# Kernel optimization log

Hardware: AMD Instinct MI355X
Metric: run time of the kernel (lower is better)

The kernel has to match this reference:

```python
import jax, jax.numpy as jnp
import numpy as np

D_MODEL = 1024
N_HEADS = 16
D_HEAD = D_MODEL // N_HEADS


def setup_inputs() -> dict:
    key = jax.random.key(0)
    ks = jax.random.split(key, 9)
    s = 1.0 / np.sqrt(D_MODEL)
    x = jax.random.normal(ks[0], (2, 2048, D_MODEL), dtype=jnp.float32)
    # torch nn.Linear stores weight [out, in]; we store [in, out] for x @ W
    Wq = jax.random.uniform(ks[1], (D_MODEL, D_MODEL), jnp.float32, -s, s)
    bq = jax.random.uniform(ks[2], (D_MODEL,), jnp.float32, -s, s)
    Wk = jax.random.uniform(ks[3], (D_MODEL, D_MODEL), jnp.float32, -s, s)
    bk = jax.random.uniform(ks[4], (D_MODEL,), jnp.float32, -s, s)
    Wv = jax.random.uniform(ks[5], (D_MODEL, D_MODEL), jnp.float32, -s, s)
    bv = jax.random.uniform(ks[6], (D_MODEL,), jnp.float32, -s, s)
    Wo = jax.random.uniform(ks[7], (D_MODEL, D_MODEL), jnp.float32, -s, s)
    bo = jax.random.uniform(ks[8], (D_MODEL,), jnp.float32, -s, s)
    return {"x": x, "Wq": Wq, "bq": bq, "Wk": Wk, "bk": bk,
            "Wv": Wv, "bv": bv, "Wo": Wo, "bo": bo}


def reference(x, Wq, bq, Wk, bk, Wv, bv, Wo, bo):
    B, S, _ = x.shape
    # project and split heads: [B, H, S, Dh]
    def split(t):
        return t.reshape(B, S, N_HEADS, D_HEAD).transpose(0, 2, 1, 3)
    Q = split(x @ Wq + bq)
    K = split(x @ Wk + bk)
    V = split(x @ Wv + bv)
    scale = 1.0 / jnp.sqrt(jnp.asarray(D_HEAD, x.dtype))
    scores = jnp.einsum('bhqd,bhkd->bhqk', Q, K) * scale  # [B,H,S,S]
    attn = jax.nn.softmax(scores, axis=-1)
    out = jnp.einsum('bhqk,bhkd->bhqd', attn, V)  # [B,H,S,Dh]
    out = out.transpose(0, 2, 1, 3).reshape(B, S, D_MODEL)
    return out @ Wo + bo
```

## Files before the change

### kernel.cpp

```cpp
#include <hip/hip_runtime.h>
#include <hip/hip_bf16.h>
#include <cmath>

#define D_MODEL 1024
#define N_HEADS 16
#define D_HEAD  64
#define BATCH   2
#define SEQ     2048
#define M_TOT   (BATCH*SEQ)
#define NELT    ((size_t)M_TOT * D_MODEL)

typedef __attribute__((ext_vector_type(8))) short short8;
typedef __attribute__((ext_vector_type(4))) float f32x4;

#define QSCALE (0.125f * 1.44269504088896f)

static __device__ __forceinline__ ushort f2bf(float f) {
    __hip_bfloat16 h = __float2bfloat16(f);
    return *reinterpret_cast<ushort*>(&h);
}

static __device__ __forceinline__ float exp2_raw(float x) {
    return __builtin_amdgcn_exp2f(x);
}

static __device__ __forceinline__ void gload_lds16(const void* g, void* l) {
    __builtin_amdgcn_global_load_lds((const __attribute__((address_space(1))) unsigned*)g,
                                     (__attribute__((address_space(3))) unsigned*)l,
                                     16, 0, 0);
}

__global__ __launch_bounds__(256)
void f32_to_bf16_kernel(const float* __restrict__ in, ushort* __restrict__ out, int n4)
{
    const int i = blockIdx.x * 256 + threadIdx.x;
    if (i < n4) {
        const float4 v = ((const float4*)in)[i];
        ushort4 u;
        u.x = f2bf(v.x); u.y = f2bf(v.y); u.z = f2bf(v.z); u.w = f2bf(v.w);
        ((ushort4*)out)[i] = u;
    }
}

__global__ __launch_bounds__(256)
void transpose_w4_kernel(const float* __restrict__ W0, const float* __restrict__ W1,
                         const float* __restrict__ W2, const float* __restrict__ W3,
                         ushort* __restrict__ Wt0)
{
    __shared__ float Ts[64][65];
    const int z = blockIdx.z;
    const float* W = (z == 0) ? W0 : (z == 1) ? W1 : (z == 2) ? W2 : W3;
    ushort* Wt = Wt0 + (size_t)z * D_MODEL * D_MODEL;

    const int t  = threadIdx.x;
    const int n0 = blockIdx.x * 64;
    const int k0 = blockIdx.y * 64;
    const int rr = t >> 4;
    const int c4 = (t & 15) * 4;

#pragma unroll
    for (int i = 0; i < 4; ++i) {
        const int r = rr + i * 16;
        const float4 v = *(const float4*)&W[(size_t)(k0 + r) * D_MODEL + n0 + c4];
        Ts[r][c4 + 0] = v.x; Ts[r][c4 + 1] = v.y;
        Ts[r][c4 + 2] = v.z; Ts[r][c4 + 3] = v.w;
    }
    __syncthreads();
#pragma unroll
    for (int i = 0; i < 4; ++i) {
        const int nn = rr + i * 16;
        ushort4 u;
        u.x = f2bf(Ts[c4 + 0][nn]); u.y = f2bf(Ts[c4 + 1][nn]);
        u.z = f2bf(Ts[c4 + 2][nn]); u.w = f2bf(Ts[c4 + 3][nn]);
        *(ushort4*)&Wt[(size_t)(n0 + nn) * D_MODEL + k0 + c4] = u;
    }
}

__global__ __launch_bounds__(256)
void gemm_qkv_mfma(const ushort* __restrict__ A, const ushort* __restrict__ Bt,
                   const float* __restrict__ bq, const float* __restrict__ bk,
                   const float* __restrict__ bv, ushort* __restrict__ QKV)
{
    __shared__ ushort As[128 * 64];
    __shared__ ushort Bs[128 * 64];

    const int t    = threadIdx.x;
    const int lane = t & 63;
    const int w    = t >> 6;
    const int wr   = w >> 1;
    const int wc   = w & 1;
    const int l16  = lane & 15;
    const int g    = lane >> 4;
    const int m0   = blockIdx.y * 128;
    const int n0   = blockIdx.x * 128;

    f32x4 acc[4][4];
#pragma unroll
    for (int i = 0; i < 4; ++i)
#pragma unroll
        for (int j = 0; j < 4; ++j) acc[i][j] = f32x4{0.f, 0.f, 0.f, 0.f};

    for (int kt = 0; kt < D_MODEL; kt += 64) {
        __syncthreads();
        const ushort* Ag = A  + (size_t)m0 * D_MODEL + kt;
        const ushort* Bg = Bt + (size_t)n0 * D_MODEL + kt;
#pragma unroll
        for (int it = 0; it < 4; ++it) {
            const int b   = (it * 256 + t) * 16;
            const int row = b >> 7;
            const int src = (b & 127) ^ ((row & 7) << 4);
            const int lof = (it * 256 + (t & ~63)) * 8;
            gload_lds16(Ag + (size_t)row * D_MODEL + (src >> 1), As + lof);
            gload_lds16(Bg + (size_t)row * D_MODEL + (src >> 1), Bs + lof);
        }
        __syncthreads();

#pragma unroll
        for (int kh = 0; kh < 2; ++kh) {
            short8 a[4], bfr[4];
#pragma unroll
            for (int fm = 0; fm < 4; ++fm) {
                const int row  = wr * 64 + fm * 16 + l16;
                const int byte = row * 128 + (((kh << 6) | (g << 4)) ^ ((row & 7) << 4));
                a[fm] = *(const short8*)((const char*)As + byte);
            }
#pragma unroll
            for (int fn = 0; fn < 4; ++fn) {
                const int row  = wc * 64 + fn * 16 + l16;
                const int byte = row * 128 + (((kh << 6) | (g << 4)) ^ ((row & 7) << 4));
                bfr[fn] = *(const short8*)((const char*)Bs + byte);
            }
#pragma unroll
            for (int fm = 0; fm < 4; ++fm)
#pragma unroll
                for (int fn = 0; fn < 4; ++fn)
                    acc[fm][fn] = __builtin_amdgcn_mfma_f32_16x16x32_bf16(a[fm], bfr[fn], acc[fm][fn], 0, 0, 0);
        }
    }

#pragma unroll
    for (int fm = 0; fm < 4; ++fm) {
        const int mb  = m0 + wr * 64 + fm * 16 + g * 4;
        const int bb  = mb >> 11;
        const int sA  = mb & (SEQ - 1);
#pragma unroll
        for (int fn = 0; fn < 4; ++fn) {
            const int n    = n0 + wc * 64 + fn * 16 + l16;
            const int proj = n >> 10;
            const int nn   = n & 1023;
            const int h    = nn >> 6;
            const int dh   = nn & 63;
            const float bn = (proj == 0) ? bq[nn] : (proj == 1) ? bk[nn] : bv[nn];
            if (proj == 2) {
                ushort4 pk;
                pk.x = f2bf(acc[fm][fn][0] + bn);
                pk.y = f2bf(acc[fm][fn][1] + bn);
                pk.z = f2bf(acc[fm][fn][2] + bn);
                pk.w = f2bf(acc[fm][fn][3] + bn);
                *(ushort4*)&QKV[2 * NELT +
                                (((size_t)(bb * N_HEADS + h)) * D_HEAD + dh) * SEQ + sA] = pk;
            } else {
                const float sc = (proj == 0) ? QSCALE : 1.0f;
                ushort* outp = QKV + (size_t)proj * NELT;
#pragma unroll
                for (int r = 0; r < 4; ++r) {
                    const float c = (acc[fm][fn][r] + bn) * sc;
                    outp[(((size_t)(bb * N_HEADS + h)) * SEQ + sA + r) * D_HEAD + dh] = f2bf(c);
                }
            }
        }
    }
}

__global__ __launch_bounds__(256)
void gemm_out_mfma(const ushort* __restrict__ A, const ushort* __restrict__ Bt,
                   const float* __restrict__ bias, float* __restrict__ outp)
{
    __shared__ ushort As[128 * 64];
    __shared__ ushort Bs[128 * 64];

    const int t    = threadIdx.x;
    const int lane = t & 63;
    const int w    = t >> 6;
    const int wr   = w >> 1;
    const int wc   = w & 1;
    const int l16  = lane & 15;
    const int g    = lane >> 4;
    const int m0   = blockIdx.y * 128;
    const int n0   = blockIdx.x * 128;

    f32x4 acc[4][4];
#pragma unroll
    for (int i = 0; i < 4; ++i)
#pragma unroll
        for (int j = 0; j < 4; ++j) acc[i][j] = f32x4{0.f, 0.f, 0.f, 0.f};

    for (int kt = 0; kt < D_MODEL; kt += 64) {
        __syncthreads();
        const ushort* Ag = A  + (size_t)m0 * D_MODEL + kt;
        const ushort* Bg = Bt + (size_t)n0 * D_MODEL + kt;
#pragma unroll
        for (int it = 0; it < 4; ++it) {
            const int b   = (it * 256 + t) * 16;
            const int row = b >> 7;
            const int src = (b & 127) ^ ((row & 7) << 4);
            const int lof = (it * 256 + (t & ~63)) * 8;
            gload_lds16(Ag + (size_t)row * D_MODEL + (src >> 1), As + lof);
            gload_lds16(Bg + (size_t)row * D_MODEL + (src >> 1), Bs + lof);
        }
        __syncthreads();

#pragma unroll
        for (int kh = 0; kh < 2; ++kh) {
            short8 a[4], bfr[4];
#pragma unroll
            for (int fm = 0; fm < 4; ++fm) {
                const int row  = wr * 64 + fm * 16 + l16;
                const int byte = row * 128 + (((kh << 6) | (g << 4)) ^ ((row & 7) << 4));
                a[fm] = *(const short8*)((const char*)As + byte);
            }
#pragma unroll
            for (int fn = 0; fn < 4; ++fn) {
                const int row  = wc * 64 + fn * 16 + l16;
                const int byte = row * 128 + (((kh << 6) | (g << 4)) ^ ((row & 7) << 4));
                bfr[fn] = *(const short8*)((const char*)Bs + byte);
            }
#pragma unroll
            for (int fm = 0; fm < 4; ++fm)
#pragma unroll
                for (int fn = 0; fn < 4; ++fn)
                    acc[fm][fn] = __builtin_amdgcn_mfma_f32_16x16x32_bf16(a[fm], bfr[fn], acc[fm][fn], 0, 0, 0);
        }
    }

#pragma unroll
    for (int fm = 0; fm < 4; ++fm) {
        const int mb = m0 + wr * 64 + fm * 16 + g * 4;
#pragma unroll
        for (int fn = 0; fn < 4; ++fn) {
            const int n  = n0 + wc * 64 + fn * 16 + l16;
            const float bn = bias[n];
#pragma unroll
            for (int r = 0; r < 4; ++r)
                outp[(size_t)(mb + r) * D_MODEL + n] = acc[fm][fn][r] + bn;
        }
    }
}

__global__ __launch_bounds__(256)
void flash_attn_mfma(const ushort* __restrict__ Q, const ushort* __restrict__ K,
                     const ushort* __restrict__ Vt, ushort* __restrict__ AO)
{
    __shared__ ushort Kl[2][64 * 64];
    __shared__ ushort Vl[2][64 * 64];
    __shared__ ushort Ps[4][2][16][80];

    const int t    = threadIdx.x;
    const int w    = t >> 6;
    const int lane = t & 63;
    const int l16  = lane & 15;
    const int g    = lane >> 4;
    const int qt   = blockIdx.x;
    const int bh   = blockIdx.y;

    const size_t qkbase = (size_t)bh * SEQ * D_HEAD;
    const ushort* Vg0 = Vt + (size_t)bh * D_HEAD * SEQ;

    short8 qf[2][2];
#pragma unroll
    for (int tt = 0; tt < 2; ++tt) {
        const int q0 = qt * 128 + w * 32 + tt * 16;
        const ushort* qp = Q + qkbase + (size_t)(q0 + l16) * D_HEAD + g * 8;
        qf[tt][0] = *(const short8*)(qp);
        qf[tt][1] = *(const short8*)(qp + 32);
    }

    f32x4 o[2][4];
    float m_r[2], l_r[2];
#pragma unroll
    for (int tt = 0; tt < 2; ++tt) {
        m_r[tt] = -INFINITY; l_r[tt] = 0.f;
#pragma unroll
        for (int d = 0; d < 4; ++d) o[tt][d] = f32x4{0.f, 0.f, 0.f, 0.f};
    }

    auto stage = [&](int ktile, int b) {
        const ushort* Kg = K + qkbase + (size_t)(ktile * 64) * D_HEAD;
        const ushort* Vg = Vg0 + ktile * 64;
#pragma unroll
        for (int it = 0; it < 2; ++it) {
            const int bb  = (it * 256 + t) * 16;
            const int row = bb >> 7;
            const int src = (bb & 127) ^ ((row & 7) << 4);
            const int lof = (it * 256 + (t & ~63)) * 8;
            gload_lds16(Kg + (size_t)row * D_HEAD + (src >> 1), &Kl[b][lof]);
            gload_lds16(Vg + (size_t)row * SEQ + (src >> 1), &Vl[b][lof]);
        }
    };

    stage(0, 0);
    __syncthreads();

    const int NT = SEQ / 64;
    for (int kt = 0; kt < NT; ++kt) {
        const int buf = kt & 1;
        if (kt + 1 < NT) stage(kt + 1, buf ^ 1);

        short8 kf[4][2];
#pragma unroll
        for (int nt = 0; nt < 4; ++nt) {
            const int row = nt * 16 + l16;
#pragma unroll
            for (int ks = 0; ks < 2; ++ks) {
                const int byte = row * 128 + (((ks * 64) | (g * 16)) ^ ((row & 7) << 4));
                kf[nt][ks] = *(const short8*)((const char*)&Kl[buf][0] + byte);
            }
        }

        f32x4 st[2][4];
#pragma unroll
        for (int tt = 0; tt < 2; ++tt)
#pragma unroll
            for (int nt = 0; nt < 4; ++nt) {
                f32x4 a = f32x4{0.f, 0.f, 0.f, 0.f};
                a = __builtin_amdgcn_mfma_f32_16x16x32_bf16(kf[nt][0], qf[tt][0], a, 0, 0, 0);
                a = __builtin_amdgcn_mfma_f32_16x16x32_bf16(kf[nt][1], qf[tt][1], a, 0, 0, 0);
                st[tt][nt] = a;
            }

#pragma unroll
        for (int tt = 0; tt < 2; ++tt) {
            float pmax = st[tt][0][0];
#pragma unroll
            for (int nt = 0; nt < 4; ++nt)
#pragma unroll
                for (int r = 0; r < 4; ++r) pmax = fmaxf(pmax, st[tt][nt][r]);
            pmax = fmaxf(pmax, __shfl_xor(pmax, 16, 64));
            pmax = fmaxf(pmax, __shfl_xor(pmax, 32, 64));

            if (__any(pmax - m_r[tt] > 8.f)) {
                const float mnew  = fmaxf(m_r[tt], pmax);
                const float alpha = exp2_raw(m_r[tt] - mnew);
                m_r[tt] = mnew;
                l_r[tt] *= alpha;
                float ar[4];
#pragma unroll
                for (int r = 0; r < 4; ++r) ar[r] = __shfl(alpha, g * 4 + r, 64);
#pragma unroll
                for (int dt = 0; dt < 4; ++dt)
#pragma unroll
                    for (int r = 0; r < 4; ++r) o[tt][dt][r] *= ar[r];
            }

            float rs = 0.f;
#pragma unroll
            for (int nt = 0; nt < 4; ++nt) {
                ushort4 pk;
#pragma unroll
                for (int r = 0; r < 4; ++r) {
                    const float p = exp2_raw(st[tt][nt][r] - m_r[tt]);
                    rs += p;
                    ((ushort*)&pk)[r] = f2bf(p);
                }
                *(ushort4*)&Ps[w][tt][l16][nt * 16 + g * 4] = pk;
            }
            rs += __shfl_xor(rs, 16, 64);
            rs += __shfl_xor(rs, 32, 64);
            l_r[tt] += rs;
        }

        short8 vf[4][2];
#pragma unroll
        for (int dt = 0; dt < 4; ++dt) {
            const int row = dt * 16 + l16;
#pragma unroll
            for (int ks = 0; ks < 2; ++ks) {
                const int byte = row * 128 + (((ks * 64) | (g * 16)) ^ ((row & 7) << 4));
                vf[dt][ks] = *(const short8*)((const char*)&Vl[buf][0] + byte);
            }
        }

#pragma unroll
        for (int tt = 0; tt < 2; ++tt)
#pragma unroll
            for (int ks = 0; ks < 2; ++ks) {
                const short8 pf = *(const short8*)&Ps[w][tt][l16][ks * 32 + g * 8];
#pragma unroll
                for (int dt = 0; dt < 4; ++dt)
                    o[tt][dt] = __builtin_amdgcn_mfma_f32_16x16x32_bf16(pf, vf[dt][ks], o[tt][dt], 0, 0, 0);
            }

        __syncthreads();
    }

    const int b = bh >> 4;
    const int h = bh & 15;
#pragma unroll
    for (int tt = 0; tt < 2; ++tt) {
        const int q0 = qt * 128 + w * 32 + tt * 16;
        float lr_row[4];
#pragma unroll
        for (int r = 0; r < 4; ++r) lr_row[r] = __shfl(l_r[tt], g * 4 + r, 64);
#pragma unroll
        for (int r = 0; r < 4; ++r) {
            const float inv = 1.f / lr_row[r];
            const size_t row = (size_t)b * SEQ + q0 + g * 4 + r;
#pragma unroll
            for (int dt = 0; dt < 4; ++dt)
                AO[row * D_MODEL + h * D_HEAD + dt * 16 + l16] = f2bf(o[tt][dt][r] * inv);
        }
    }
}

extern "C" void kernel_launch(void* const* d_in, const int* in_sizes, int n_in,
                              void* d_out, int out_size, void* d_ws, size_t ws_size,
                              hipStream_t stream)
{
    const float* x  = (const float*)d_in[0];
    const float* Wq = (const float*)d_in[1];
    const float* bq = (const float*)d_in[2];
    const float* Wk = (const float*)d_in[3];
    const float* bk = (const float*)d_in[4];
    const float* Wv = (const float*)d_in[5];
    const float* bv = (const float*)d_in[6];
    const float* Wo = (const float*)d_in[7];
    const float* bo = (const float*)d_in[8];
    float* out = (float*)d_out;

    const size_t WELT = (size_t)D_MODEL * D_MODEL;
    ushort* xb  = (ushort*)d_ws;
    ushort* Wqt = xb + NELT;
    ushort* Wot = Wqt + 3 * WELT;
    ushort* Qb  = xb + 2 * NELT;
    ushort* Kb  = Qb + NELT;
    ushort* Vtb = Kb + NELT;
    ushort* AOb = xb + 5 * NELT;

    f32_to_bf16_kernel<<<dim3(M_TOT * D_MODEL / 4 / 256), 256, 0, stream>>>(x, xb, M_TOT * D_MODEL / 4);
    transpose_w4_kernel<<<dim3(D_MODEL / 64, D_MODEL / 64, 4), 256, 0, stream>>>(Wq, Wk, Wv, Wo, Wqt);
    gemm_qkv_mfma<<<dim3(3 * D_MODEL / 128, M_TOT / 128), 256, 0, stream>>>(xb, Wqt, bq, bk, bv, Qb);
    flash_attn_mfma<<<dim3(SEQ / 128, BATCH * N_HEADS), 256, 0, stream>>>(Qb, Kb, Vtb, AOb);
    gemm_out_mfma<<<dim3(D_MODEL / 128, M_TOT / 128), 256, 0, stream>>>(AOb, Wot, bo, out);
}
```

Before: 144.0 us.

## Merge prep kernels, enlarge attention KV tiles, shrink output GEMM M-tile

The x conversion and the weight transposes now run in one prep launch, with z==4 blocks handling x in 4096-float4 slabs. Flash attention stages 128-key K/V tiles per iteration, processed in two 64-key halves, which halves the barrier and loop count at the cost of doubled LDS buffers. The P staging buffer now uses a swizzled layout in place of padding. The output GEMM uses 64x128 tiles so the launch has twice as many blocks for better CU occupancy, trading away some operand reuse.

```diff
diff --git a/kernel.cpp b/kernel.cpp
--- a/kernel.cpp
+++ b/kernel.cpp
@@ -31,28 +31,31 @@
 }
 
 __global__ __launch_bounds__(256)
-void f32_to_bf16_kernel(const float* __restrict__ in, ushort* __restrict__ out, int n4)
-{
-    const int i = blockIdx.x * 256 + threadIdx.x;
-    if (i < n4) {
-        const float4 v = ((const float4*)in)[i];
-        ushort4 u;
-        u.x = f2bf(v.x); u.y = f2bf(v.y); u.z = f2bf(v.z); u.w = f2bf(v.w);
-        ((ushort4*)out)[i] = u;
-    }
-}
-
-__global__ __launch_bounds__(256)
-void transpose_w4_kernel(const float* __restrict__ W0, const float* __restrict__ W1,
-                         const float* __restrict__ W2, const float* __restrict__ W3,
-                         ushort* __restrict__ Wt0)
+void prep_kernel(const float* __restrict__ x,
+                 const float* __restrict__ W0, const float* __restrict__ W1,
+                 const float* __restrict__ W2, const float* __restrict__ W3,
+                 ushort* __restrict__ xb, ushort* __restrict__ Wt0)
 {
     __shared__ float Ts[64][65];
     const int z = blockIdx.z;
+    const int t = threadIdx.x;
+
+    if (z == 4) {
+        const int slab = blockIdx.y * 16 + blockIdx.x;
+#pragma unroll
+        for (int u = 0; u < 16; ++u) {
+            const int i = slab * 4096 + u * 256 + t;
+            const float4 v = ((const float4*)x)[i];
+            ushort4 uo;
+            uo.x = f2bf(v.x); uo.y = f2bf(v.y); uo.z = f2bf(v.z); uo.w = f2bf(v.w);
+            ((ushort4*)xb)[i] = uo;
+        }
+        return;
+    }
+
     const float* W = (z == 0) ? W0 : (z == 1) ? W1 : (z == 2) ? W2 : W3;
     ushort* Wt = Wt0 + (size_t)z * D_MODEL * D_MODEL;
 
-    const int t  = threadIdx.x;
     const int n0 = blockIdx.x * 64;
     const int k0 = blockIdx.y * 64;
     const int rr = t >> 4;
@@ -176,69 +179,74 @@
 void gemm_out_mfma(const ushort* __restrict__ A, const ushort* __restrict__ Bt,
                    const float* __restrict__ bias, float* __restrict__ outp)
 {
-    __shared__ ushort As[128 * 64];
+    __shared__ ushort As[64 * 64];
     __shared__ ushort Bs[128 * 64];
 
     const int t    = threadIdx.x;
     const int lane = t & 63;
     const int w    = t >> 6;
-    const int wr   = w >> 1;
-    const int wc   = w & 1;
     const int l16  = lane & 15;
     const int g    = lane >> 4;
-    const int m0   = blockIdx.y * 128;
+    const int m0   = blockIdx.y * 64;
     const int n0   = blockIdx.x * 128;
 
-    f32x4 acc[4][4];
+    f32x4 acc[4][2];
 #pragma unroll
     for (int i = 0; i < 4; ++i)
 #pragma unroll
-        for (int j = 0; j < 4; ++j) acc[i][j] = f32x4{0.f, 0.f, 0.f, 0.f};
+        for (int j = 0; j < 2; ++j) acc[i][j] = f32x4{0.f, 0.f, 0.f, 0.f};
 
     for (int kt = 0; kt < D_MODEL; kt += 64) {
         __syncthreads();
         const ushort* Ag = A  + (size_t)m0 * D_MODEL + kt;
         const ushort* Bg = Bt + (size_t)n0 * D_MODEL + kt;
+#pragma unroll
+        for (int it = 0; it < 2; ++it) {
+            const int b   = (it * 256 + t) * 16;
+            const int row = b >> 7;
+            const int src = (b & 127) ^ ((row & 7) << 4);
+            const int lof = (it * 256 + (t & ~63)) * 8;
+            gload_lds16(Ag + (size_t)row * D_MODEL + (src >> 1), As + lof);
+        }
 #pragma unroll
         for (int it = 0; it < 4; ++it) {
             const int b   = (it * 256 + t) * 16;
             const int row = b >> 7;
             const int src = (b & 127) ^ ((row & 7) << 4);
             const int lof = (it * 256 + (t & ~63)) * 8;
-            gload_lds16(Ag + (size_t)row * D_MODEL + (src >> 1), As + lof);
             gload_lds16(Bg + (size_t)row * D_MODEL + (src >> 1), Bs + lof);
         }
         __syncthreads();
 
 #pragma unroll
         for (int kh = 0; kh < 2; ++kh) {
-            short8 a[4], bfr[4];
+            short8 a[4], bfr[2];
 #pragma unroll
             for (int fm = 0; fm < 4; ++fm) {
-                const int row  = wr * 64 + fm * 16 + l16;
+                const int row  = fm * 16 + l16;
                 const int byte = row * 128 + (((kh << 6) | (g << 4)) ^ ((row & 7) << 4));
                 a[fm] = *(const short8*)((const char*)As + byte);
             }
 #pragma unroll
-            for (int fn = 0; fn < 4; ++fn) {
-                const int row  = wc * 64 + fn * 16 + l16;
+            for (int fn = 0; fn < 2; ++fn) {
+                const int row  = w * 32 + fn * 16 + l16;
                 const int byte = row * 128 + (((kh << 6) | (g << 4)) ^ ((row & 7) << 4));
                 bfr[fn] = *(const short8*)((const char*)Bs + byte);
             }
 #pragma unroll
             for (int fm = 0; fm < 4; ++fm)
 #pragma unroll
-                for (int fn = 0; fn < 4; ++fn)
+                for (int fn = 0; fn < 2; ++fn)
                     acc[fm][fn] = __builtin_amdgcn_mfma_f32_16x16x32_bf16(a[fm], bfr[fn], acc[fm][fn], 0, 0, 0);
         }
     }
 
 #pragma unroll
     for (int fm = 0; fm < 4; ++fm) {
-        const int mb = m0 + wr * 64 + fm * 16 + g * 4;
-#pragma unroll
-        for (int fn = 0; fn < 4; ++fn) {
-            const int n  = n0 + wc * 64 + fn * 16 + l16;
+        const int mb = m0 + fm * 16 + g * 4;
+#pragma unroll
+        for (int fn = 0; fn < 2; ++fn) {
+            const int n  = n0 + w * 32 + fn * 16 + l16;
             const float bn = bias[n];
 #pragma unroll
             for (int r = 0; r < 4; ++r)
@@ -251,9 +259,9 @@
 void flash_attn_mfma(const ushort* __restrict__ Q, const ushort* __restrict__ K,
                      const ushort* __restrict__ Vt, ushort* __restrict__ AO)
 {
-    __shared__ ushort Kl[2][64 * 64];
-    __shared__ ushort Vl[2][64 * 64];
-    __shared__ ushort Ps[4][2][16][80];
+    __shared__ ushort Kl[2][128 * 64];
+    __shared__ ushort Vl[2][64 * 128];
+    __shared__ ushort Ps[4][16 * 64];
 
     const int t    = threadIdx.x;
     const int w    = t >> 6;
@@ -285,110 +293,115 @@
     }
 
     auto stage = [&](int ktile, int b) {
-        const ushort* Kg = K + qkbase + (size_t)(ktile * 64) * D_HEAD;
-        const ushort* Vg = Vg0 + ktile * 64;
-#pragma unroll
-        for (int it = 0; it < 2; ++it) {
-            const int bb  = (it * 256 + t) * 16;
-            const int row = bb >> 7;
-            const int src = (bb & 127) ^ ((row & 7) << 4);
-            const int lof = (it * 256 + (t & ~63)) * 8;
-            gload_lds16(Kg + (size_t)row * D_HEAD + (src >> 1), &Kl[b][lof]);
-            gload_lds16(Vg + (size_t)row * SEQ + (src >> 1), &Vl[b][lof]);
+        const ushort* Kg = K + qkbase + (size_t)(ktile * 128) * D_HEAD;
+        const ushort* Vg = Vg0 + ktile * 128;
+#pragma unroll
+        for (int it = 0; it < 4; ++it) {
+            const int bb   = (it * 256 + t) * 16;
+            const int lof  = (it * 256 + (t & ~63)) * 8;
+            const int rowK = bb >> 7;
+            const int srcK = (bb & 127) ^ ((rowK & 7) << 4);
+            gload_lds16(Kg + (size_t)rowK * D_HEAD + (srcK >> 1), &Kl[b][lof]);
+            const int rowV = bb >> 8;
+            const int srcV = (bb & 255) ^ ((rowV & 15) << 4);
+            gload_lds16(Vg + (size_t)rowV * SEQ + (srcV >> 1), &Vl[b][lof]);
         }
     };
 
     stage(0, 0);
     __syncthreads();
 
-    const int NT = SEQ / 64;
+    const int NT = SEQ / 128;
     for (int kt = 0; kt < NT; ++kt) {
         const int buf = kt & 1;
         if (kt + 1 < NT) stage(kt + 1, buf ^ 1);
 
-        short8 kf[4][2];
-#pragma unroll
-        for (int nt = 0; nt < 4; ++nt) {
-            const int row = nt * 16 + l16;
-#pragma unroll
-            for (int ks = 0; ks < 2; ++ks) {
-                const int byte = row * 128 + (((ks * 64) | (g * 16)) ^ ((row & 7) << 4));
-                kf[nt][ks] = *(const short8*)((const char*)&Kl[buf][0] + byte);
-            }
-        }
-
-        f32x4 st[2][4];
-#pragma unroll
-        for (int tt = 0; tt < 2; ++tt)
+#pragma unroll
+        for (int h2 = 0; h2 < 2; ++h2) {
+            short8 kf[4][2];
 #pragma unroll
             for (int nt = 0; nt < 4; ++nt) {
-                f32x4 a = f32x4{0.f, 0.f, 0.f, 0.f};
-                a = __builtin_amdgcn_mfma_f32_16x16x32_bf16(kf[nt][0], qf[tt][0], a, 0, 0, 0);
-                a = __builtin_amdgcn_mfma_f32_16x16x32_bf16(kf[nt][1], qf[tt][1], a, 0, 0, 0);
-                st[tt][nt] = a;
-            }
-
-#pragma unroll
-        for (int tt = 0; tt < 2; ++tt) {
-            float pmax = st[tt][0][0];
-#pragma unroll
-            for (int nt = 0; nt < 4; ++nt)
-#pragma unroll
-                for (int r = 0; r < 4; ++r) pmax = fmaxf(pmax, st[tt][nt][r]);
-            pmax = fmaxf(pmax, __shfl_xor(pmax, 16, 64));
-            pmax = fmaxf(pmax, __shfl_xor(pmax, 32, 64));
-
-            if (__any(pmax - m_r[tt] > 8.f)) {
-                const float mnew  = fmaxf(m_r[tt], pmax);
-                const float alpha = exp2_raw(m_r[tt] - mnew);
-                m_r[tt] = mnew;
-                l_r[tt] *= alpha;
-                float ar[4];
-#pragma unroll
-                for (int r = 0; r < 4; ++r) ar[r] = __shfl(alpha, g * 4 + r, 64);
-#pragma unroll
-                for (int dt = 0; dt < 4; ++dt)
-#pragma unroll
-                    for (int r = 0; r < 4; ++r) o[tt][dt][r] *= ar[r];
-            }
-
-            float rs = 0.f;
-#pragma unroll
-            for (int nt = 0; nt < 4; ++nt) {
-                ushort4 pk;
-#pragma unroll
-                for (int r = 0; r < 4; ++r) {
-                    const float p = exp2_raw(st[tt][nt][r] - m_r[tt]);
-                    rs += p;
-                    ((ushort*)&pk)[r] = f2bf(p);
-                }
-                *(ushort4*)&Ps[w][tt][l16][nt * 16 + g * 4] = pk;
-            }
-            rs += __shfl_xor(rs, 16, 64);
-            rs += __shfl_xor(rs, 32, 64);
-            l_r[tt] += rs;
-        }
-
-        short8 vf[4][2];
-#pragma unroll
-        for (int dt = 0; dt < 4; ++dt) {
-            const int row = dt * 16 + l16;
-#pragma unroll
-            for (int ks = 0; ks < 2; ++ks) {
-                const int byte = row * 128 + (((ks * 64) | (g * 16)) ^ ((row & 7) << 4));
-                vf[dt][ks] = *(const short8*)((const char*)&Vl[buf][0] + byte);
-            }
-        }
-
-#pragma unroll
-        for (int tt = 0; tt < 2; ++tt)
-#pragma unroll
-            for (int ks = 0; ks < 2; ++ks) {
-                const short8 pf = *(const short8*)&Ps[w][tt][l16][ks * 32 + g * 8];
-#pragma unroll
-                for (int dt = 0; dt < 4; ++dt)
-                    o[tt][dt] = __builtin_amdgcn_mfma_f32_16x16x32_bf16(pf, vf[dt][ks], o[tt][dt], 0, 0, 0);
-            }
+                const int row = h2 * 64 + nt * 16 + l16;
+#pragma unroll
+                for (int ks = 0; ks < 2; ++ks) {
+                    const int byte = row * 128 + (((ks * 64) | (g * 16)) ^ ((row & 7) << 4));
+                    kf[nt][ks] = *(const short8*)((const char*)&Kl[buf][0] + byte);
+                }
+            }
+
+            short8 vf[4][2];
+#pragma unroll
+            for (int dt = 0; dt < 4; ++dt) {
+                const int row = dt * 16 + l16;
+#pragma unroll
+                for (int ks = 0; ks < 2; ++ks) {
+                    const int byte = row * 256 + ((h2 * 128 + ks * 64 + g * 16) ^ ((row & 15) << 4));
+                    vf[dt][ks] = *(const short8*)((const char*)&Vl[buf][0] + byte);
+                }
+            }
+
+            f32x4 st[2][4];
+#pragma unroll
+            for (int tt = 0; tt < 2; ++tt)
+#pragma unroll
+                for (int nt = 0; nt < 4; ++nt) {
+                    f32x4 a = f32x4{0.f, 0.f, 0.f, 0.f};
+                    a = __builtin_amdgcn_mfma_f32_16x16x32_bf16(kf[nt][0], qf[tt][0], a, 0, 0, 0);
+                    a = __builtin_amdgcn_mfma_f32_16x16x32_bf16(kf[nt][1], qf[tt][1], a, 0, 0, 0);
+                    st[tt][nt] = a;
+                }
+
+#pragma unroll
+            for (int tt = 0; tt < 2; ++tt) {
+                float pmax = st[tt][0][0];
+#pragma unroll
+                for (int nt = 0; nt < 4; ++nt)
+#pragma unroll
+                    for (int r = 0; r < 4; ++r) pmax = fmaxf(pmax, st[tt][nt][r]);
+                pmax = fmaxf(pmax, __shfl_xor(pmax, 16, 64));
+                pmax = fmaxf(pmax, __shfl_xor(pmax, 32, 64));
+
+                if (__any(pmax - m_r[tt] > 8.f)) {
+                    const float mnew  = fmaxf(m_r[tt], pmax);
+                    const float alpha = exp2_raw(m_r[tt] - mnew);
+                    m_r[tt] = mnew;
+                    l_r[tt] *= alpha;
+                    float ar[4];
+#pragma unroll
+                    for (int r = 0; r < 4; ++r) ar[r] = __shfl(alpha, g * 4 + r, 64);
+#pragma unroll
+                    for (int dt = 0; dt < 4; ++dt)
+#pragma unroll
+                        for (int r = 0; r < 4; ++r) o[tt][dt][r] *= ar[r];
+                }
+
+                float rs = 0.f;
+#pragma unroll
+                for (int nt = 0; nt < 4; ++nt) {
+                    ushort4 pk;
+#pragma unroll
+                    for (int r = 0; r < 4; ++r) {
+                        const float p = exp2_raw(st[tt][nt][r] - m_r[tt]);
+                        rs += p;
+                        ((ushort*)&pk)[r] = f2bf(p);
+                    }
+                    const int pb = (nt * 32 + g * 8) ^ ((l16 & 7) << 4);
+                    *(ushort4*)((char*)&Ps[w][0] + l16 * 128 + pb) = pk;
+                }
+                rs += __shfl_xor(rs, 16, 64);
+                rs += __shfl_xor(rs, 32, 64);
+                l_r[tt] += rs;
+
+#pragma unroll
+                for (int ks = 0; ks < 2; ++ks) {
+                    const int rb = (ks * 64 + g * 16) ^ ((l16 & 7) << 4);
+                    const short8 pf = *(const short8*)((const char*)&Ps[w][0] + l16 * 128 + rb);
+#pragma unroll
+                    for (int dt = 0; dt < 4; ++dt)
+                        o[tt][dt] = __builtin_amdgcn_mfma_f32_16x16x32_bf16(pf, vf[dt][ks], o[tt][dt], 0, 0, 0);
+                }
+            }
+        }
 
         __syncthreads();
     }
@@ -436,9 +449,8 @@
     ushort* Vtb = Kb + NELT;
     ushort* AOb = xb + 5 * NELT;
 
-    f32_to_bf16_kernel<<<dim3(M_TOT * D_MODEL / 4 / 256), 256, 0, stream>>>(x, xb, M_TOT * D_MODEL / 4);
-    transpose_w4_kernel<<<dim3(D_MODEL / 64, D_MODEL / 64, 4), 256, 0, stream>>>(Wq, Wk, Wv, Wo, Wqt);
+    prep_kernel<<<dim3(D_MODEL / 64, D_MODEL / 64, 5), 256, 0, stream>>>(x, Wq, Wk, Wv, Wo, xb, Wqt);
     gemm_qkv_mfma<<<dim3(3 * D_MODEL / 128, M_TOT / 128), 256, 0, stream>>>(xb, Wqt, bq, bk, bv, Qb);
     flash_attn_mfma<<<dim3(SEQ / 128, BATCH * N_HEADS), 256, 0, stream>>>(Qb, Kb, Vtb, AOb);
-    gemm_out_mfma<<<dim3(D_MODEL / 128, M_TOT / 128), 256, 0, stream>>>(AOb, Wot, bo, out);
-}
+    gemm_out_mfma<<<dim3(D_MODEL / 128, M_TOT / 64), 256, 0, stream>>>(AOb, Wot, bo, out);
+}
```

Measured after the change: 129.8 us. 1.11x faster.
